# Kernel tuning notes

Measured on AMD Instinct MI355X. Metric: run time of the kernel, lower is better.

Reference implementation:

```python
import jax, jax.numpy as jnp
import numpy as np

B, C_FEAT, C_COND, C_KEY, H, W = 4, 256, 256, 32, 64, 64


def setup_inputs() -> dict:
    key = jax.random.key(0)
    ks = jax.random.split(key, 8)
    s = 0.02
    return {
        "features": jax.random.normal(ks[0], (B, C_FEAT, H, W), jnp.float32),
        "conditions": jax.random.normal(ks[1], (B, C_COND, H, W), jnp.float32),
        "Wq": jax.random.normal(ks[2], (C_KEY, C_COND), jnp.float32) * s,
        "bq": jnp.zeros((C_KEY,), jnp.float32),
        "Wk": jax.random.normal(ks[3], (C_KEY, C_FEAT), jnp.float32) * s,
        "bk": jnp.zeros((C_KEY,), jnp.float32),
        "Wv": jax.random.normal(ks[4], (C_FEAT, C_FEAT), jnp.float32) * s,
        "bv": jnp.zeros((C_FEAT,), jnp.float32),
        "gamma": jnp.zeros((1,), jnp.float32),
    }


def reference(features, conditions, Wq, bq, Wk, bk, Wv, bv, gamma):
    b, c, h, w = features.shape
    n = h * w
    feat = features.reshape(b, c, n)            # [B, C, N]
    cond = conditions.reshape(b, cond_c := conditions.shape[1], n)
    # 1x1 convs == per-pixel linear projections
    q = jnp.einsum('kc,bcn->bnk', Wq, cond) + bq          # [B, N, Ck]
    k = jnp.einsum('kc,bcn->bkn', Wk, feat) + bk[:, None]  # [B, Ck, N]
    v = jnp.einsum('oc,bcn->bon', Wv, feat) + bv[:, None]  # [B, C, N]
    energy = jnp.einsum('bik,bkj->bij', q, k)             # [B, N, N]
    attn = jax.nn.softmax(energy, axis=-1)
    out = jnp.einsum('bcj,bij->bci', v, attn)             # [B, C, N]
    out = out.reshape(b, c, h, w)
    return gamma * out + features
```

## Files before the change

### kernel.cpp

```cpp
#include <hip/hip_runtime.h>

typedef __bf16 bf16_t;
typedef __bf16 bf16x2 __attribute__((ext_vector_type(2)));
typedef __bf16 bf16x4 __attribute__((ext_vector_type(4)));
typedef __bf16 bf16x8 __attribute__((ext_vector_type(8)));
typedef float f32x4 __attribute__((ext_vector_type(4)));
typedef unsigned u32;
typedef unsigned u32x4 __attribute__((ext_vector_type(4)));

#define N_PIX 4096
#define CFEAT 256
#define CKEY 32
#define NBATCH 4

#if __has_builtin(__builtin_amdgcn_exp2f)
#define EXP2(x) __builtin_amdgcn_exp2f(x)
#else
#define EXP2(x) exp2f(x)
#endif

static __device__ __forceinline__ f32x4 mfma16(bf16x8 a, bf16x8 b, f32x4 c) {
    return __builtin_amdgcn_mfma_f32_16x16x32_bf16(a, b, c, 0, 0, 0);
}

static __device__ __forceinline__ void glds16(const void* g, void* l) {
    __builtin_amdgcn_global_load_lds(
        (const __attribute__((address_space(1))) void*)g,
        (__attribute__((address_space(3))) void*)l, 16, 0, 0);
}

static __device__ __forceinline__ u32 pk2(float lo, float hi) {
    bf16x2 t; t[0] = (bf16_t)lo; t[1] = (bf16_t)hi;
    return __builtin_bit_cast(u32, t);
}

static __device__ __forceinline__ void xpose4(u32 &x, u32 &y) {
#if __has_builtin(__builtin_amdgcn_permlane32_swap) && __has_builtin(__builtin_amdgcn_permlane16_swap)
    auto r32 = __builtin_amdgcn_permlane32_swap(x, y, false, false);
    auto r16 = __builtin_amdgcn_permlane16_swap(r32[0], r32[1], false, false);
    x = r16[0]; y = r16[1];
#else
    const int lane = threadIdx.x & 63;
    const int g = lane >> 4, ln = lane & 15;
    const int i0 = ln + ((g & 1) << 5);
    const int i2 = i0 + 16;
    u32 xs0 = (u32)__shfl((int)x, i0), ys0 = (u32)__shfl((int)y, i0);
    u32 xs2 = (u32)__shfl((int)x, i2), ys2 = (u32)__shfl((int)y, i2);
    x = (g < 2) ? xs0 : ys0;
    y = (g < 2) ? xs2 : ys2;
#endif
}

static __device__ __forceinline__ void softmax_tile(
    const bf16x8 kf[4], bf16x8 qf, bf16x8 ones,
    f32x4 &accsum, bf16x8 &pa0, bf16x8 &pa1)
{
    f32x4 zero = {0.f, 0.f, 0.f, 0.f};
    f32x4 st[4];
#pragma unroll
    for (int jt = 0; jt < 4; ++jt) st[jt] = mfma16(kf[jt], qf, zero);
    float ex[16];
#pragma unroll
    for (int jt = 0; jt < 4; ++jt)
#pragma unroll
        for (int r = 0; r < 4; ++r) ex[jt * 4 + r] = EXP2(st[jt][r]);
    u32 a0 = pk2(ex[0],  ex[1]),  a1 = pk2(ex[2],  ex[3]);
    u32 b0 = pk2(ex[4],  ex[5]),  b1 = pk2(ex[6],  ex[7]);
    u32 c0 = pk2(ex[8],  ex[9]),  c1 = pk2(ex[10], ex[11]);
    u32 d0 = pk2(ex[12], ex[13]), d1 = pk2(ex[14], ex[15]);
    xpose4(a0, b0); xpose4(a1, b1);
    xpose4(c0, d0); xpose4(c1, d1);
    u32x4 w0 = {a0, a1, b0, b1};
    u32x4 w1 = {c0, c1, d0, d1};
    pa0 = __builtin_bit_cast(bf16x8, w0);
    pa1 = __builtin_bit_cast(bf16x8, w1);
    accsum = mfma16(ones, pa0, accsum);
    accsum = mfma16(ones, pa1, accsum);
}

__global__ __launch_bounds__(256) void proj_kernel(
    const float* __restrict__ Wq, const float* __restrict__ bq, const float* __restrict__ cond,
    const float* __restrict__ Wk, const float* __restrict__ bk, const float* __restrict__ feat,
    const float* __restrict__ Wv, const float* __restrict__ bv,
    bf16_t* __restrict__ Qt, bf16_t* __restrict__ Kt, bf16_t* __restrict__ Vv)
{
    __shared__ __attribute__((aligned(16))) bf16_t T[64][40];
    const int lane = threadIdx.x & 63, wave = threadIdx.x >> 6;
    const int g = lane >> 4, ln = lane & 15;
    const int bid = blockIdx.x;
    f32x4 zero = {0.f, 0.f, 0.f, 0.f};

    if (bid < 512) {
        const bool isK = (bid >= 256);
        const int idx = bid & 255;
        const int xt = idx & 63;
        const int b  = idx >> 6;
        const float* W    = isK ? Wk : Wq;
        const float* bias = isK ? bk : bq;
        const float* X  = (isK ? feat : cond) + (size_t)b * CFEAT * N_PIX;
        bf16_t*      Yt = (isK ? Kt : Qt) + (size_t)b * N_PIX * CKEY;
        const float qscale = isK ? 1.0f : 1.4426950408889634f;

        const int m_base = (wave & 1) * 16;
        const int n_loc  = (wave >> 1) * 32;
        const int n_base = xt * 64 + n_loc;

        f32x4 acc[2] = {zero, zero};
        for (int k0 = 0; k0 < CFEAT; k0 += 32) {
            bf16x8 a;
            const float* wp = W + (size_t)(m_base + ln) * CFEAT + k0 + g * 8;
#pragma unroll
            for (int j = 0; j < 8; ++j) a[j] = (bf16_t)wp[j];
#pragma unroll
            for (int nt = 0; nt < 2; ++nt) {
                const float* xp = X + (size_t)(k0 + g * 8) * N_PIX + n_base + nt * 16 + ln;
                bf16x8 bfr;
#pragma unroll
                for (int j = 0; j < 8; ++j) bfr[j] = (bf16_t)xp[(size_t)j * N_PIX];
                acc[nt] = mfma16(a, bfr, acc[nt]);
            }
        }
#pragma unroll
        for (int nt = 0; nt < 2; ++nt)
#pragma unroll
            for (int r = 0; r < 4; ++r) {
                const int ck = m_base + g * 4 + r;
                T[n_loc + nt * 16 + ln][ck] = (bf16_t)((acc[nt][r] + bias[ck]) * qscale);
            }
        __syncthreads();
        const int n  = threadIdx.x >> 2;
        const int sg = threadIdx.x & 3;
        bf16x8 row = *(const bf16x8*)&T[n][sg * 8];
        *(bf16x8*)&Yt[(size_t)(xt * 64 + n) * CKEY + sg * 8] = row;
    } else {
        const int idx = bid - 512;
        const int xt = idx & 127;
        const int b  = idx >> 7;
        const int n_base = xt * 32;
        const int c_wave = wave * 64;
        const float* Xb = feat + (size_t)b * CFEAT * N_PIX;
        bf16_t*      Vb = Vv + (size_t)b * CFEAT * N_PIX;

        f32x4 acc[4][2];
#pragma unroll
        for (int mt = 0; mt < 4; ++mt) { acc[mt][0] = zero; acc[mt][1] = zero; }

        for (int k0 = 0; k0 < CFEAT; k0 += 32) {
            bf16x8 bfr[2];
#pragma unroll
            for (int nt = 0; nt < 2; ++nt) {
                const float* xp = Xb + (size_t)(k0 + g * 8) * N_PIX + n_base + nt * 16 + ln;
#pragma unroll
                for (int j = 0; j < 8; ++j) bfr[nt][j] = (bf16_t)xp[(size_t)j * N_PIX];
            }
#pragma unroll
            for (int mt = 0; mt < 4; ++mt) {
                const float* wp = Wv + (size_t)(c_wave + mt * 16 + ln) * CFEAT + k0 + g * 8;
                bf16x8 a;
#pragma unroll
                for (int j = 0; j < 8; ++j) a[j] = (bf16_t)wp[j];
                acc[mt][0] = mfma16(a, bfr[0], acc[mt][0]);
                acc[mt][1] = mfma16(a, bfr[1], acc[mt][1]);
            }
        }
#pragma unroll
        for (int mt = 0; mt < 4; ++mt)
#pragma unroll
            for (int nt = 0; nt < 2; ++nt)
#pragma unroll
                for (int r = 0; r < 4; ++r) {
                    const int m = c_wave + mt * 16 + g * 4 + r;
                    const int n = n_base + nt * 16 + ln;
                    Vb[(size_t)m * N_PIX + n] = (bf16_t)(acc[mt][nt][r] + bv[m]);
                }
    }
}

__global__ __launch_bounds__(256, 2) void pv_kernel(
    const bf16_t* __restrict__ Qt, const bf16_t* __restrict__ Kt,
    const bf16_t* __restrict__ V,
    const float* __restrict__ features, const float* __restrict__ gamma,
    float* __restrict__ out)
{
    __shared__ __attribute__((aligned(16))) bf16_t Vlds[4][128 * 64];

    const int lane = threadIdx.x & 63, wave = threadIdx.x >> 6;
    const int g = lane >> 4, ln = lane & 15;
    const int b = blockIdx.z;
    const int i_base = blockIdx.y * 64 + wave * 16;
    const int c_base = blockIdx.x * 128;

    const bf16_t* Qb = Qt + (size_t)b * N_PIX * CKEY;
    const bf16_t* Kb = Kt + (size_t)b * N_PIX * CKEY;
    const bf16_t* Vb = V + (size_t)b * CFEAT * N_PIX;

    const int s0 = wave * 256 + lane, s1 = s0 + 64, s2 = s0 + 128, s3 = s0 + 192;
    const int sc0 = s0 >> 3, sj0 = (s0 & 7) ^ (sc0 & 7);
    const int sc1 = s1 >> 3, sj1 = (s1 & 7) ^ (sc1 & 7);
    const int sc2 = s2 >> 3, sj2 = (s2 & 7) ^ (sc2 & 7);
    const int sc3 = s3 >> 3, sj3 = (s3 & 7) ^ (sc3 & 7);
    const bf16_t* vg0 = Vb + (size_t)(c_base + sc0) * N_PIX + sj0 * 8;
    const bf16_t* vg1 = Vb + (size_t)(c_base + sc1) * N_PIX + sj1 * 8;
    const bf16_t* vg2 = Vb + (size_t)(c_base + sc2) * N_PIX + sj2 * 8;
    const bf16_t* vg3 = Vb + (size_t)(c_base + sc3) * N_PIX + sj3 * 8;

    const bf16x8 qf = *(const bf16x8*)&Qb[(size_t)(i_base + ln) * CKEY + g * 8];

    bf16x8 ones;
#pragma unroll
    for (int j = 0; j < 8; ++j) ones[j] = (bf16_t)1.0f;

    f32x4 zero = {0.f, 0.f, 0.f, 0.f};
    f32x4 acc[8] = {zero, zero, zero, zero, zero, zero, zero, zero};
    f32x4 accsum = zero;

    bf16x8 kfA[4], kfB[4];
    bf16x8 pa0c, pa1c;

    {
        bf16x8 kf0[4];
#pragma unroll
        for (int jt = 0; jt < 4; ++jt)
            kf0[jt] = *(const bf16x8*)&Kb[(size_t)(jt * 16 + ln) * CKEY + g * 8];
        asm volatile("" ::: "memory");
        glds16(vg0, &Vlds[0][wave * 2048]);
        glds16(vg1, &Vlds[0][wave * 2048 + 512]);
        glds16(vg2, &Vlds[0][wave * 2048 + 1024]);
        glds16(vg3, &Vlds[0][wave * 2048 + 1536]);
        glds16(vg0 + 64, &Vlds[1][wave * 2048]);
        glds16(vg1 + 64, &Vlds[1][wave * 2048 + 512]);
        glds16(vg2 + 64, &Vlds[1][wave * 2048 + 1024]);
        glds16(vg3 + 64, &Vlds[1][wave * 2048 + 1536]);
#pragma unroll
        for (int jt = 0; jt < 4; ++jt)
            kfA[jt] = *(const bf16x8*)&Kb[(size_t)(64 + jt * 16 + ln) * CKEY + g * 8];
        softmax_tile(kf0, qf, ones, accsum, pa0c, pa1c);
        asm volatile("s_waitcnt vmcnt(8)" ::: "memory");
        __builtin_amdgcn_s_barrier();
        asm volatile("" ::: "memory");
    }

#define PV_ITER(NN, KFU, KFN)                                                  \
  {                                                                            \
    const int nn = (NN);                                                       \
    const bf16_t* Vt = &Vlds[nn & 3][0];                                       \
    bf16x8 vf[16];                                                             \
    _Pragma("unroll")                                                          \
    for (int ct = 0; ct < 8; ++ct) {                                           \
      const int c = ct * 16 + ln;                                              \
      vf[2 * ct]     = *(const bf16x8*)&Vt[(c * 8 + ( g      ^ (c & 7))) * 8]; \
      vf[2 * ct + 1] = *(const bf16x8*)&Vt[(c * 8 + ((4 + g) ^ (c & 7))) * 8]; \
    }                                                                          \
    const int jq2 = ((nn + 2) & 63) * 64;                                      \
    _Pragma("unroll")                                                          \
    for (int jt = 0; jt < 4; ++jt)                                             \
      KFN[jt] = *(const bf16x8*)&Kb[(size_t)(jq2 + jt * 16 + ln) * CKEY + g * 8]; \
    asm volatile("" ::: "memory");     \
    const int jn = (nn * 64 + 128) & (N_PIX - 1);                              \
    bf16_t* ldst = &Vlds[(nn + 2) & 3][wave * 2048];                           \
    glds16(vg0 + jn, ldst);                                                    \
    glds16(vg1 + jn, ldst + 512);                                              \
    glds16(vg2 + jn, ldst + 1024);                                             \
    glds16(vg3 + jn, ldst + 1536);                                             \
    bf16x8 pa0n, pa1n;                                                         \
    const bool live = (nn < 63);                                               \
    if (live) softmax_tile(KFU, qf, ones, accsum, pa0n, pa1n);                 \
    asm volatile("s_waitcnt vmcnt(8)" ::: "memory");                           \
    __builtin_amdgcn_s_barrier();                                              \
    asm volatile("" ::: "memory");                                             \
    __builtin_amdgcn_s_setprio(1);                                             \
    _Pragma("unroll")                                                          \
    for (int ct = 0; ct < 8; ++ct) {                                           \
      acc[ct] = mfma16(vf[2 * ct],     pa0c, acc[ct]);                         \
      acc[ct] = mfma16(vf[2 * ct + 1], pa1c, acc[ct]);                         \
    }                                                                          \
    __builtin_amdgcn_s_setprio(0);                                             \
    if (live) { pa0c = pa0n; pa1c = pa1n; }                                    \
  }

    for (int n2 = 0; n2 < 32; ++n2) {
        PV_ITER(2 * n2,     kfA, kfB);
        PV_ITER(2 * n2 + 1, kfB, kfA);
    }
#undef PV_ITER

    const float s_lane = gamma[0] / accsum[0];

#pragma unroll
    for (int ct = 0; ct < 8; ++ct)
#pragma unroll
        for (int r = 0; r < 4; ++r) {
            const int c = c_base + ct * 16 + g * 4 + r;
            const int i = i_base + ln;
            const size_t idx = ((size_t)b * CFEAT + c) * N_PIX + i;
            out[idx] = s_lane * acc[ct][r] + features[idx];
        }
}

extern "C" void kernel_launch(void* const* d_in, const int* in_sizes, int n_in,
                              void* d_out, int out_size, void* d_ws, size_t ws_size,
                              hipStream_t stream) {
    const float* features   = (const float*)d_in[0];
    const float* conditions = (const float*)d_in[1];
    const float* Wq  = (const float*)d_in[2];
    const float* bq  = (const float*)d_in[3];
    const float* Wk  = (const float*)d_in[4];
    const float* bk  = (const float*)d_in[5];
    const float* Wv  = (const float*)d_in[6];
    const float* bv  = (const float*)d_in[7];
    const float* gam = (const float*)d_in[8];
    float* out = (float*)d_out;

    bf16_t* Qt = (bf16_t*)d_ws;
    bf16_t* Kt = Qt + (size_t)NBATCH * N_PIX * CKEY;
    bf16_t* Vw = Kt + (size_t)NBATCH * N_PIX * CKEY;

    proj_kernel<<<dim3(1024, 1, 1), 256, 0, stream>>>(
        Wq, bq, conditions, Wk, bk, features, Wv, bv, Qt, Kt, Vw);
    pv_kernel<<<dim3(2, N_PIX / 64, NBATCH), 256, 0, stream>>>(
        Qt, Kt, Vw, features, gam, out);
}
```

Before: 169.4 us.

## Restructure attention so each block covers all channels and shares probabilities via LDS

The PV kernel now gives each block 32 query pixels and all 256 channels, instead of 64 queries by 128 channels. Two waves compute the exponentiated scores and write them to LDS, and all four waves read them back for the PV MFMAs over a 64-channel slice each. This removes the duplicated QK^T and exp work that was done once per channel half, and it walks keys in 32-wide steps. The cost is extra LDS traffic, lgkmcnt waits, work imbalance between the softmax waves and the others, and a grid of 512 blocks instead of 512 with a different tile shape.

```diff
diff --git a/kernel.cpp b/kernel.cpp
--- a/kernel.cpp
+++ b/kernel.cpp
@@ -2,7 +2,6 @@
 
 typedef __bf16 bf16_t;
 typedef __bf16 bf16x2 __attribute__((ext_vector_type(2)));
-typedef __bf16 bf16x4 __attribute__((ext_vector_type(4)));
 typedef __bf16 bf16x8 __attribute__((ext_vector_type(8)));
 typedef float f32x4 __attribute__((ext_vector_type(4)));
 typedef unsigned u32;
@@ -51,31 +50,25 @@
 #endif
 }
 
-static __device__ __forceinline__ void softmax_tile(
-    const bf16x8 kf[4], bf16x8 qf, bf16x8 ones,
-    f32x4 &accsum, bf16x8 &pa0, bf16x8 &pa1)
+static __device__ __forceinline__ void softmax_tile32(
+    const bf16x8 kf[2], bf16x8 qf, bf16x8 ones,
+    f32x4 &accsum, bf16x8 &pa0)
 {
     f32x4 zero = {0.f, 0.f, 0.f, 0.f};
-    f32x4 st[4];
-#pragma unroll
-    for (int jt = 0; jt < 4; ++jt) st[jt] = mfma16(kf[jt], qf, zero);
-    float ex[16];
-#pragma unroll
-    for (int jt = 0; jt < 4; ++jt)
+    f32x4 st[2];
+#pragma unroll
+    for (int jt = 0; jt < 2; ++jt) st[jt] = mfma16(kf[jt], qf, zero);
+    float ex[8];
+#pragma unroll
+    for (int jt = 0; jt < 2; ++jt)
 #pragma unroll
         for (int r = 0; r < 4; ++r) ex[jt * 4 + r] = EXP2(st[jt][r]);
-    u32 a0 = pk2(ex[0],  ex[1]),  a1 = pk2(ex[2],  ex[3]);
-    u32 b0 = pk2(ex[4],  ex[5]),  b1 = pk2(ex[6],  ex[7]);
-    u32 c0 = pk2(ex[8],  ex[9]),  c1 = pk2(ex[10], ex[11]);
-    u32 d0 = pk2(ex[12], ex[13]), d1 = pk2(ex[14], ex[15]);
+    u32 a0 = pk2(ex[0], ex[1]), a1 = pk2(ex[2], ex[3]);
+    u32 b0 = pk2(ex[4], ex[5]), b1 = pk2(ex[6], ex[7]);
     xpose4(a0, b0); xpose4(a1, b1);
-    xpose4(c0, d0); xpose4(c1, d1);
     u32x4 w0 = {a0, a1, b0, b1};
-    u32x4 w1 = {c0, c1, d0, d1};
     pa0 = __builtin_bit_cast(bf16x8, w0);
-    pa1 = __builtin_bit_cast(bf16x8, w1);
     accsum = mfma16(ones, pa0, accsum);
-    accsum = mfma16(ones, pa1, accsum);
 }
 
 __global__ __launch_bounds__(256) void proj_kernel(
@@ -182,119 +175,128 @@
     const float* __restrict__ features, const float* __restrict__ gamma,
     float* __restrict__ out)
 {
-    __shared__ __attribute__((aligned(16))) bf16_t Vlds[4][128 * 64];
+    __shared__ __attribute__((aligned(16))) bf16_t Vlds[4][8192];
+    __shared__ __attribute__((aligned(16))) bf16_t Plds[2][1024];
+    __shared__ float Llds[32];
 
     const int lane = threadIdx.x & 63, wave = threadIdx.x >> 6;
     const int g = lane >> 4, ln = lane & 15;
-    const int b = blockIdx.z;
-    const int i_base = blockIdx.y * 64 + wave * 16;
-    const int c_base = blockIdx.x * 128;
+    const int b = blockIdx.y;
+    const int i_base = blockIdx.x * 32;
+    const bool sm = (wave < 2);
 
     const bf16_t* Qb = Qt + (size_t)b * N_PIX * CKEY;
     const bf16_t* Kb = Kt + (size_t)b * N_PIX * CKEY;
     const bf16_t* Vb = V + (size_t)b * CFEAT * N_PIX;
 
-    const int s0 = wave * 256 + lane, s1 = s0 + 64, s2 = s0 + 128, s3 = s0 + 192;
-    const int sc0 = s0 >> 3, sj0 = (s0 & 7) ^ (sc0 & 7);
-    const int sc1 = s1 >> 3, sj1 = (s1 & 7) ^ (sc1 & 7);
-    const int sc2 = s2 >> 3, sj2 = (s2 & 7) ^ (sc2 & 7);
-    const int sc3 = s3 >> 3, sj3 = (s3 & 7) ^ (sc3 & 7);
-    const bf16_t* vg0 = Vb + (size_t)(c_base + sc0) * N_PIX + sj0 * 8;
-    const bf16_t* vg1 = Vb + (size_t)(c_base + sc1) * N_PIX + sj1 * 8;
-    const bf16_t* vg2 = Vb + (size_t)(c_base + sc2) * N_PIX + sj2 * 8;
-    const bf16_t* vg3 = Vb + (size_t)(c_base + sc3) * N_PIX + sj3 * 8;
-
-    const bf16x8 qf = *(const bf16x8*)&Qb[(size_t)(i_base + ln) * CKEY + g * 8];
+    const bf16_t* vgp[4];
+#pragma unroll
+    for (int q = 0; q < 4; ++q) {
+        const int s = q * 256 + wave * 64 + lane;
+        vgp[q] = Vb + (size_t)(s >> 2) * N_PIX + (s & 3) * 8;
+    }
+
+#define STAGE(BUF, JOFF)                                                     \
+    { _Pragma("unroll") for (int q = 0; q < 4; ++q)                          \
+        glds16(vgp[q] + (JOFF), &Vlds[BUF][(q * 256 + wave * 64) * 8]); }
+
+#define LOADK(DST, JQ)                                                       \
+    { _Pragma("unroll") for (int jt = 0; jt < 2; ++jt)                       \
+        DST[jt] = *(const bf16x8*)&Kb[(size_t)((JQ) + jt * 16 + ln) * CKEY + g * 8]; }
+
+#define PWRITE(SLOT, PA0)                                                    \
+    { *(bf16x8*)&Plds[SLOT][(wave * 16 + ln) * 32 + g * 8] = PA0; }
+
+    bf16x8 qf = {};
+    if (sm) qf = *(const bf16x8*)&Qb[(size_t)(i_base + wave * 16 + ln) * CKEY + g * 8];
 
     bf16x8 ones;
 #pragma unroll
     for (int j = 0; j < 8; ++j) ones[j] = (bf16_t)1.0f;
 
     f32x4 zero = {0.f, 0.f, 0.f, 0.f};
-    f32x4 acc[8] = {zero, zero, zero, zero, zero, zero, zero, zero};
+    f32x4 acc[4][2];
+#pragma unroll
+    for (int ct = 0; ct < 4; ++ct) { acc[ct][0] = zero; acc[ct][1] = zero; }
     f32x4 accsum = zero;
 
-    bf16x8 kfA[4], kfB[4];
-    bf16x8 pa0c, pa1c;
-
-    {
-        bf16x8 kf0[4];
-#pragma unroll
-        for (int jt = 0; jt < 4; ++jt)
-            kf0[jt] = *(const bf16x8*)&Kb[(size_t)(jt * 16 + ln) * CKEY + g * 8];
-        asm volatile("" ::: "memory");
-        glds16(vg0, &Vlds[0][wave * 2048]);
-        glds16(vg1, &Vlds[0][wave * 2048 + 512]);
-        glds16(vg2, &Vlds[0][wave * 2048 + 1024]);
-        glds16(vg3, &Vlds[0][wave * 2048 + 1536]);
-        glds16(vg0 + 64, &Vlds[1][wave * 2048]);
-        glds16(vg1 + 64, &Vlds[1][wave * 2048 + 512]);
-        glds16(vg2 + 64, &Vlds[1][wave * 2048 + 1024]);
-        glds16(vg3 + 64, &Vlds[1][wave * 2048 + 1536]);
-#pragma unroll
-        for (int jt = 0; jt < 4; ++jt)
-            kfA[jt] = *(const bf16x8*)&Kb[(size_t)(64 + jt * 16 + ln) * CKEY + g * 8];
-        softmax_tile(kf0, qf, ones, accsum, pa0c, pa1c);
-        asm volatile("s_waitcnt vmcnt(8)" ::: "memory");
-        __builtin_amdgcn_s_barrier();
-        asm volatile("" ::: "memory");
+    bf16x8 kfA[2], kfB[2];
+
+    if (sm) LOADK(kfA, 0);
+    asm volatile("" ::: "memory");
+    STAGE(0, 0);
+    STAGE(1, 32);
+    if (sm) {
+        bf16x8 pa0;
+        softmax_tile32(kfA, qf, ones, accsum, pa0);
+        PWRITE(0, pa0);
+        LOADK(kfA, 32);
     }
-
-#define PV_ITER(NN, KFU, KFN)                                                  \
-  {                                                                            \
-    const int nn = (NN);                                                       \
-    const bf16_t* Vt = &Vlds[nn & 3][0];                                       \
-    bf16x8 vf[16];                                                             \
-    _Pragma("unroll")                                                          \
-    for (int ct = 0; ct < 8; ++ct) {                                           \
-      const int c = ct * 16 + ln;                                              \
-      vf[2 * ct]     = *(const bf16x8*)&Vt[(c * 8 + ( g      ^ (c & 7))) * 8]; \
-      vf[2 * ct + 1] = *(const bf16x8*)&Vt[(c * 8 + ((4 + g) ^ (c & 7))) * 8]; \
-    }                                                                          \
-    const int jq2 = ((nn + 2) & 63) * 64;                                      \
-    _Pragma("unroll")                                                          \
-    for (int jt = 0; jt < 4; ++jt)                                             \
-      KFN[jt] = *(const bf16x8*)&Kb[(size_t)(jq2 + jt * 16 + ln) * CKEY + g * 8]; \
-    asm volatile("" ::: "memory");     \
-    const int jn = (nn * 64 + 128) & (N_PIX - 1);                              \
-    bf16_t* ldst = &Vlds[(nn + 2) & 3][wave * 2048];                           \
-    glds16(vg0 + jn, ldst);                                                    \
-    glds16(vg1 + jn, ldst + 512);                                              \
-    glds16(vg2 + jn, ldst + 1024);                                             \
-    glds16(vg3 + jn, ldst + 1536);                                             \
-    bf16x8 pa0n, pa1n;                                                         \
-    const bool live = (nn < 63);                                               \
-    if (live) softmax_tile(KFU, qf, ones, accsum, pa0n, pa1n);                 \
-    asm volatile("s_waitcnt vmcnt(8)" ::: "memory");                           \
-    __builtin_amdgcn_s_barrier();                                              \
-    asm volatile("" ::: "memory");                                             \
-    __builtin_amdgcn_s_setprio(1);                                             \
-    _Pragma("unroll")                                                          \
-    for (int ct = 0; ct < 8; ++ct) {                                           \
-      acc[ct] = mfma16(vf[2 * ct],     pa0c, acc[ct]);                         \
-      acc[ct] = mfma16(vf[2 * ct + 1], pa1c, acc[ct]);                         \
-    }                                                                          \
-    __builtin_amdgcn_s_setprio(0);                                             \
-    if (live) { pa0c = pa0n; pa1c = pa1n; }                                    \
+    __syncthreads();
+
+#define PV_ITER(NN, KU, KN)                                                  \
+  {                                                                          \
+    const int nn = (NN);                                                     \
+    const bf16_t* Vt = &Vlds[nn & 3][0];                                     \
+    bf16x8 vf[4];                                                            \
+    _Pragma("unroll")                                                        \
+    for (int ct = 0; ct < 4; ++ct)                                           \
+      vf[ct] = *(const bf16x8*)&Vt[(wave * 64 + ct * 16 + ln) * 32 + g * 8]; \
+    const bf16_t* Pr = &Plds[nn & 1][0];                                     \
+    bf16x8 pf[2];                                                            \
+    _Pragma("unroll")                                                        \
+    for (int it = 0; it < 2; ++it)                                           \
+      pf[it] = *(const bf16x8*)&Pr[(it * 16 + ln) * 32 + g * 8];             \
+    const bool live = (nn < 127);                                            \
+    if (sm && live) LOADK(KN, ((nn + 2) & 127) * 32);                        \
+    asm volatile("" ::: "memory");   \
+    STAGE((nn + 2) & 3, ((nn * 32 + 64) & (N_PIX - 1)));                     \
+    if (sm && live) {                                                        \
+      bf16x8 pa0;                                                            \
+      softmax_tile32(KU, qf, ones, accsum, pa0);                             \
+      PWRITE((nn + 1) & 1, pa0);                                             \
+    }                                                                        \
+    if (sm) { asm volatile("s_waitcnt vmcnt(6)" ::: "memory"); }             \
+    else    { asm volatile("s_waitcnt vmcnt(4)" ::: "memory"); }             \
+    asm volatile("s_waitcnt lgkmcnt(0)" ::: "memory");                       \
+    __builtin_amdgcn_s_barrier();                                            \
+    asm volatile("" ::: "memory");                                           \
+    __builtin_amdgcn_s_setprio(1);                                           \
+    _Pragma("unroll")                                                        \
+    for (int ct = 0; ct < 4; ++ct) {                                         \
+      acc[ct][0] = mfma16(vf[ct], pf[0], acc[ct][0]);                        \
+      acc[ct][1] = mfma16(vf[ct], pf[1], acc[ct][1]);                        \
+    }                                                                        \
+    __builtin_amdgcn_s_setprio(0);                                           \
   }
 
-    for (int n2 = 0; n2 < 32; ++n2) {
+    for (int n2 = 0; n2 < 64; ++n2) {
         PV_ITER(2 * n2,     kfA, kfB);
         PV_ITER(2 * n2 + 1, kfB, kfA);
     }
 #undef PV_ITER
 
-    const float s_lane = gamma[0] / accsum[0];
-
-#pragma unroll
-    for (int ct = 0; ct < 8; ++ct)
-#pragma unroll
-        for (int r = 0; r < 4; ++r) {
-            const int c = c_base + ct * 16 + g * 4 + r;
-            const int i = i_base + ln;
-            const size_t idx = ((size_t)b * CFEAT + c) * N_PIX + i;
-            out[idx] = s_lane * acc[ct][r] + features[idx];
-        }
+    if (sm && g == 0) Llds[wave * 16 + ln] = accsum[0];
+    __syncthreads();
+    const float gam = gamma[0];
+    float sc2[2];
+#pragma unroll
+    for (int it = 0; it < 2; ++it) sc2[it] = gam / Llds[it * 16 + ln];
+
+#pragma unroll
+    for (int ct = 0; ct < 4; ++ct)
+#pragma unroll
+        for (int it = 0; it < 2; ++it)
+#pragma unroll
+            for (int r = 0; r < 4; ++r) {
+                const int c = wave * 64 + ct * 16 + g * 4 + r;
+                const int i = i_base + it * 16 + ln;
+                const size_t idx = ((size_t)b * CFEAT + c) * N_PIX + i;
+                out[idx] = sc2[it] * acc[ct][it][r] + features[idx];
+            }
+#undef STAGE
+#undef LOADK
+#undef PWRITE
 }
 
 extern "C" void kernel_launch(void* const* d_in, const int* in_sizes, int n_in,
@@ -317,6 +319,6 @@
 
     proj_kernel<<<dim3(1024, 1, 1), 256, 0, stream>>>(
         Wq, bq, conditions, Wk, bk, features, Wv, bv, Qt, Kt, Vw);
-    pv_kernel<<<dim3(2, N_PIX / 64, NBATCH), 256, 0, stream>>>(
+    pv_kernel<<<dim3(128, NBATCH, 1), 256, 0, stream>>>(
         Qt, Kt, Vw, features, gam, out);
 }
```

Measured after the change: 191.0 us. +12.7%, slower.
